# Optimization experiments

Measured on AMD Instinct MI355X. Metric: run time of the kernel, lower is better.

The kernel has to match this reference:

```python
import jax, jax.numpy as jnp
import numpy as np

N_A = 50000; N_B = 50000          # nodes per type
FD = 8; BINS = 32; EMB = 16       # discrete features, bins, per-feature embed dim
HID = 64; ZD = 32                 # hidden_dim, embed_dim
E = 800000                        # edges per relation (avg degree 16)


def setup_inputs() -> dict:
    key = jax.random.key(0)
    ks = iter(jax.random.split(key, 64))
    def nrm(shape, s=0.05):
        return jax.random.normal(next(ks), shape, jnp.float32) * s
    def ri(shape, hi):
        return jax.random.randint(next(ks), shape, 0, hi, dtype=jnp.int32)
    inp = {
        'x_A': ri((N_A, FD), BINS),
        'x_B': ri((N_B, FD), BINS),
        'ei_ab': ri((2, E), N_A),   # src in A, dst in B (N_A == N_B)
        'ei_ba': ri((2, E), N_B),
        'ei_aa': ri((2, E), N_A),
        # per-feature embedding tables [FD, BINS, EMB]
        'emb_A': nrm((FD, BINS, EMB)), 'emb_B': nrm((FD, BINS, EMB)),
        # pre_lin per node type (in = FD*EMB)
        'pre_W_A': nrm((FD * EMB, HID)), 'pre_b_A': nrm((HID,)),
        'pre_W_B': nrm((FD * EMB, HID)), 'pre_b_B': nrm((HID,)),
        # SAGEConv per relation: lin_l (on aggregated msgs, with bias), lin_r (root, no bias)
        'sage_l_W_ab': nrm((HID, HID)), 'sage_l_b_ab': nrm((HID,)), 'sage_r_W_ab': nrm((HID, HID)),
        'sage_l_W_ba': nrm((HID, HID)), 'sage_l_b_ba': nrm((HID,)), 'sage_r_W_ba': nrm((HID, HID)),
        'sage_l_W_aa': nrm((HID, HID)), 'sage_l_b_aa': nrm((HID,)), 'sage_r_W_aa': nrm((HID, HID)),
        # lin_proj per node type
        'proj_W_A': nrm((HID, ZD)), 'proj_b_A': nrm((ZD,)),
        'proj_W_B': nrm((HID, ZD)), 'proj_b_B': nrm((ZD,)),
        # feature heads per node type -> FD*BINS logits
        'head_W_A': nrm((ZD, FD * BINS)), 'head_b_A': nrm((FD * BINS,)),
        'head_W_B': nrm((ZD, FD * BINS)), 'head_b_B': nrm((FD * BINS,)),
        # bilinear edge decoders per relation: W [1, ZD, ZD], bias [1]
        'bil_W_ab': nrm((1, ZD, ZD)), 'bil_b_ab': nrm((1,)),
        'bil_W_ba': nrm((1, ZD, ZD)), 'bil_b_ba': nrm((1,)),
        'bil_W_aa': nrm((1, ZD, ZD)), 'bil_b_aa': nrm((1,)),
    }
    return inp


def _segment_mean(vals, idx, n):
    s = jax.ops.segment_sum(vals, idx, num_segments=n)
    c = jax.ops.segment_sum(jnp.ones((vals.shape[0], 1), vals.dtype), idx, num_segments=n)
    return s / jnp.maximum(c, 1.0)


def _sage(x_src, x_dst, ei, Wl, bl, Wr):
    # SAGEConv: lin_l(mean_{j in N(i)} x_j) + lin_r(x_i)
    m = _segment_mean(x_src[ei[0]], ei[1], x_dst.shape[0])
    return m @ Wl + bl + x_dst @ Wr


def _embed(x, emb):
    # emb: [FD, BINS, EMB]; x: [N, FD] ints -> [N, FD*EMB]
    e = emb[jnp.arange(FD)[None, :], x]            # [N, FD, EMB]
    return e.reshape(x.shape[0], FD * EMB)


def _bilinear(zs, zd, W, b):
    # nn.Bilinear: out_o = zs^T W_o zd + b_o ; here out dim 1, squeeze
    return (jnp.einsum('ei,oij,ej->eo', zs, W, zd) + b)[:, 0]


def _forward(x_A, x_B, ei_ab, ei_ba, ei_aa,
             emb_A, emb_B, pre_W_A, pre_b_A, pre_W_B, pre_b_B,
             sage_l_W_ab, sage_l_b_ab, sage_r_W_ab,
             sage_l_W_ba, sage_l_b_ba, sage_r_W_ba,
             sage_l_W_aa, sage_l_b_aa, sage_r_W_aa,
             proj_W_A, proj_b_A, proj_W_B, proj_b_B,
             head_W_A, head_b_A, head_W_B, head_b_B,
             bil_W_ab, bil_b_ab, bil_W_ba, bil_b_ba, bil_W_aa, bil_b_aa):
    # feature encoder + pre_lin + relu
    x0_A = jax.nn.relu(_embed(x_A, emb_A) @ pre_W_A + pre_b_A)
    x0_B = jax.nn.relu(_embed(x_B, emb_B) @ pre_W_B + pre_b_B)
    # HeteroConv(SAGEConv per relation, aggr='mean' over relations per dst type)
    h_B = _sage(x0_A, x0_B, ei_ab, sage_l_W_ab, sage_l_b_ab, sage_r_W_ab)
    h_A = (_sage(x0_B, x0_A, ei_ba, sage_l_W_ba, sage_l_b_ba, sage_r_W_ba)
           + _sage(x0_A, x0_A, ei_aa, sage_l_W_aa, sage_l_b_aa, sage_r_W_aa)) * 0.5
    # projection
    z_A = jax.nn.relu(h_A @ proj_W_A + proj_b_A)
    z_B = jax.nn.relu(h_B @ proj_W_B + proj_b_B)
    # feature decode
    fl_A = (z_A @ head_W_A + head_b_A).reshape(-1, FD, BINS)
    fl_B = (z_B @ head_W_B + head_b_B).reshape(-1, FD, BINS)
    # edge decode (bilinear on gathered endpoint embeddings)
    s_ab = _bilinear(z_A[ei_ab[0]], z_B[ei_ab[1]], bil_W_ab, bil_b_ab)
    s_ba = _bilinear(z_B[ei_ba[0]], z_A[ei_ba[1]], bil_W_ba, bil_b_ba)
    s_aa = _bilinear(z_A[ei_aa[0]], z_A[ei_aa[1]], bil_W_aa, bil_b_aa)
    return (z_A, z_B, fl_A, fl_B, s_ab, s_ba, s_aa)


def reference(x_A, x_B, ei_ab, ei_ba, ei_aa,
              emb_A, emb_B, pre_W_A, pre_b_A, pre_W_B, pre_b_B,
              sage_l_W_ab, sage_l_b_ab, sage_r_W_ab,
              sage_l_W_ba, sage_l_b_ba, sage_r_W_ba,
              sage_l_W_aa, sage_l_b_aa, sage_r_W_aa,
              proj_W_A, proj_b_A, proj_W_B, proj_b_B,
              head_W_A, head_b_A, head_W_B, head_b_B,
              bil_W_ab, bil_b_ab, bil_W_ba, bil_b_ba, bil_W_aa, bil_b_aa):
    return _forward(x_A, x_B, ei_ab, ei_ba, ei_aa,
                    emb_A, emb_B, pre_W_A, pre_b_A, pre_W_B, pre_b_B,
                    sage_l_W_ab, sage_l_b_ab, sage_r_W_ab,
                    sage_l_W_ba, sage_l_b_ba, sage_r_W_ba,
                    sage_l_W_aa, sage_l_b_aa, sage_r_W_aa,
                    proj_W_A, proj_b_A, proj_W_B, proj_b_B,
                    head_W_A, head_b_A, head_W_B, head_b_B,
                    bil_W_ab, bil_b_ab, bil_W_ba, bil_b_ba, bil_W_aa, bil_b_aa)
```

## Files before the change

kernel.cpp:

```cpp
#include <hip/hip_runtime.h>

typedef unsigned short u16;
typedef unsigned int u32;
typedef __attribute__((ext_vector_type(8))) short short8;
typedef __attribute__((ext_vector_type(4))) float f32x4;

constexpr int NA = 50000, NB = 50000;
constexpr int EMB = 16, HID = 64;
constexpr int NE = 800000;
constexpr int NBKT = 782;
constexpr int CAPB = 1536;
constexpr int EPB = 2048;
constexpr int BPR = (NE + EPB - 1) / EPB;
constexpr int MSB = 3 * BPR;

#define MFMA16(a, b, c) __builtin_amdgcn_mfma_f32_16x16x32_bf16(a, b, c, 0, 0, 0)

__device__ inline u16 f2bf(float f) {
  u32 b = __float_as_uint(f);
  return (u16)((b + 0x7FFFu + ((b >> 16) & 1u)) >> 16);
}
__device__ inline float bfl(u32 u) { return __uint_as_float(u << 16); }
__device__ inline float bfh(u32 u) { return __uint_as_float(u & 0xFFFF0000u); }
__device__ inline float bfs(u16 u) { return __uint_as_float((u32)u << 16); }

__global__ void __launch_bounds__(256) k_pre(
    const float* __restrict__ embA, const float* __restrict__ embB,
    const float* __restrict__ preWA, const float* __restrict__ preWB,
    float* __restrict__ T,
    const float* __restrict__ Wr_ba, const float* __restrict__ Wr_aa,
    const float* __restrict__ Wl_ba, const float* __restrict__ Wl_aa,
    const float* __restrict__ Wl_ab, const float* __restrict__ Wr_ab,
    const float* __restrict__ bl_ba, const float* __restrict__ bl_aa,
    const float* __restrict__ projWA, const float* __restrict__ projWB,
    const float* __restrict__ headWA, const float* __restrict__ headWB,
    const float* __restrict__ bilW_ba, const float* __restrict__ bilW_aa,
    const float* __restrict__ bilW_ab,
    u16* __restrict__ frag, float* __restrict__ bhA,
    const int* __restrict__ ei_ab, const int* __restrict__ ei_ba,
    const int* __restrict__ ei_aa, int* __restrict__ gcur,
    u32* __restrict__ buckets) {
  __shared__ int hist[NBKT];
  __shared__ int wcur[NBKT];
  int blk = blockIdx.x;
  int t = threadIdx.x;

  if (blk < MSB) {
    int rel = blk / BPR;
    int lb = blk - rel * BPR;
    const int* ei = rel == 0 ? ei_ab : (rel == 1 ? ei_ba : ei_aa);
    int e0 = lb * EPB;
    int n = min(EPB, NE - e0);
    for (int i = t; i < NBKT; i += 256) hist[i] = 0;
    __syncthreads();
    for (int i = t; i < n; i += 256) {
      int dstn = ei[NE + e0 + i];
      atomicAdd(&hist[dstn >> 6], 1);
    }
    __syncthreads();
    for (int i = t; i < NBKT; i += 256) {
      int c = hist[i];
      wcur[i] = (c > 0) ? atomicAdd(&gcur[rel * NBKT + i], c) : 0;
    }
    __syncthreads();
    for (int i = t; i < n; i += 256) {
      int src = ei[e0 + i];
      int dstn = ei[NE + e0 + i];
      int b = dstn >> 6;
      int pos = atomicAdd(&wcur[b], 1);
      if (pos < CAPB)
        buckets[(size_t)(rel * NBKT + b) * CAPB + pos] =
            ((u32)src << 6) | (u32)(dstn & 63);
    }
    return;
  }

  if (blk < MSB + 128) {
    int id = (blk - MSB) * 256 + t;
    int type = id >> 14;
    int rem = id & 16383;
    int col = rem >> 8;
    int fdbin = rem & 255;
    int fd = fdbin >> 5;
    const float* emb = type ? embB : embA;
    const float* W = type ? preWB : preWA;
    const float* e = emb + fdbin * EMB;
    const float* w = W + (fd * EMB) * HID + col;
    float s = 0.f;
#pragma unroll
    for (int j = 0; j < EMB; ++j) s += e[j] * w[j * HID];
    T[id] = s;
    return;
  }

  int tid = (blk - MSB - 128) * 256 + t;
  if (tid >= 86 * 64) {
    int i = tid - 86 * 64;
    if (i < 64) bhA[i] = 0.5f * (bl_ba[i] + bl_aa[i]);
    return;
  }
  int f = tid >> 6, lane = tid & 63;
  int nidx = lane & 15, quad = lane >> 4;
  u16* dst = frag + (size_t)f * 512 + lane * 8;
#pragma unroll
  for (int j = 0; j < 8; ++j) {
    int kq = quad * 8 + j;
    float v;
    if (f < 24) {
      int s = f >> 2, nt = f & 3, k = s * 32 + kq, c = nt * 16 + nidx;
      v = (k < 64) ? 0.5f * (Wr_ba[k * 64 + c] + Wr_aa[k * 64 + c])
          : (k < 128) ? 0.5f * Wl_ba[(k - 64) * 64 + c]
                      : 0.5f * Wl_aa[(k - 128) * 64 + c];
    } else if (f < 28) {
      int g = f - 24, k = (g >> 1) * 32 + kq, c = (g & 1) * 16 + nidx;
      v = projWA[k * 32 + c];
    } else if (f < 44) {
      int c = (f - 28) * 16 + nidx;
      v = headWA[kq * 256 + c];
    } else if (f < 46) {
      int i2 = (f - 44) * 16 + nidx;
      v = bilW_ba[i2 * 32 + kq];
    } else if (f < 48) {
      int i2 = (f - 46) * 16 + nidx;
      v = bilW_aa[i2 * 32 + kq];
    } else if (f < 64) {
      int g = f - 48, s = g >> 2, nt = g & 3, k = s * 32 + kq, c = nt * 16 + nidx;
      v = (k < 64) ? Wr_ab[k * 64 + c] : Wl_ab[(k - 64) * 64 + c];
    } else if (f < 68) {
      int g = f - 64, k = (g >> 1) * 32 + kq, c = (g & 1) * 16 + nidx;
      v = projWB[k * 32 + c];
    } else if (f < 84) {
      int c = (f - 68) * 16 + nidx;
      v = headWB[kq * 256 + c];
    } else {
      int i2 = (f - 84) * 16 + nidx;
      v = bilW_ab[i2 * 32 + kq];
    }
    dst[j] = f2bf(v);
  }
}

__global__ void __launch_bounds__(256) k_x0(const int* __restrict__ xA,
                                            const int* __restrict__ xB,
                                            const float* __restrict__ T,
                                            const float* __restrict__ biasA,
                                            const float* __restrict__ biasB,
                                            u16* __restrict__ x0A,
                                            u16* __restrict__ x0B) {
  extern __shared__ float Tl[];
  int blk = blockIdx.x;
  int type = blk >= 782;
  int lb = type ? blk - 782 : blk;
  const int* x = type ? xB : xA;
  const float* Tt = T + (type ? 16384 : 0);
  const float* bias = type ? biasB : biasA;
  u16* x0 = type ? x0B : x0A;
  const int N = NA;

  const float4* Tg = (const float4*)Tt;
  float4* Ts = (float4*)Tl;
  for (int i = threadIdx.x; i < 4096; i += 256) {
    int col = i >> 6, b4 = i & 63;
    Ts[col * 64 + ((b4 + 2 * (col >> 4)) & 63)] = Tg[i];
  }
  __syncthreads();
  int t = threadIdx.x;
  int r = t >> 2, q = t & 3;
  int row = lb * 64 + r;
  bool valid = row < N;
  int arow = valid ? row : (N - 1);
  const int4* xp = (const int4*)(x + arow * 8);
  int4 xa = xp[0], xb = xp[1];
  int bins[8] = {xa.x, xa.y, xa.z, xa.w, xb.x, xb.y, xb.z, xb.w};
  int c0 = q * 16;
  float acc[16];
#pragma unroll
  for (int j = 0; j < 16; ++j) acc[j] = bias[c0 + j];
#pragma unroll
  for (int fd = 0; fd < 8; ++fd) {
    int sb = ((fd * 32 + bins[fd]) + 8 * q) & 255;
#pragma unroll
    for (int j = 0; j < 16; ++j) acc[j] += Tl[(c0 + j) * 256 + sb];
  }
  if (valid) {
    u32 p[8];
#pragma unroll
    for (int j = 0; j < 8; ++j) {
      u16 lo = f2bf(fmaxf(acc[2 * j], 0.f));
      u16 hi = f2bf(fmaxf(acc[2 * j + 1], 0.f));
      p[j] = (u32)lo | ((u32)hi << 16);
    }
    u32* o = (u32*)(x0 + (size_t)row * 64 + c0);
    *(uint4*)o = *(uint4*)&p[0];
    *((uint4*)o + 1) = *(uint4*)&p[4];
  }
}

__global__ void __launch_bounds__(256) k_meansort_all(
    const u32* __restrict__ buckets, const int* __restrict__ cur,
    const u16* __restrict__ x0A, const u16* __restrict__ x0B,
    u16* __restrict__ mab, u16* __restrict__ mba, u16* __restrict__ maa) {
  __shared__ u32 ebuf[CAPB];
  __shared__ u16 csr[CAPB];
  __shared__ int dcnt[64], doff[64], wcur[64];
  int blk = blockIdx.x;
  int rel = blk / NBKT;
  int lb = blk - rel * NBKT;
  int t = threadIdx.x;
  const u16* x0 = (rel == 1) ? x0B : x0A;
  u16* out = rel == 0 ? mab : (rel == 1 ? mba : maa);
  int n = min(cur[blk], CAPB);
  const u32* bk = buckets + (size_t)blk * CAPB;
  if (t < 64) dcnt[t] = 0;
  __syncthreads();
  for (int i = t; i < n; i += 256) {
    u32 v = bk[i];
    ebuf[i] = v;
    atomicAdd(&dcnt[v & 63], 1);
  }
  __syncthreads();
  if (t == 0) {
    int s = 0;
#pragma unroll
    for (int d = 0; d < 64; ++d) {
      doff[d] = s;
      wcur[d] = s;
      s += dcnt[d];
    }
  }
  __syncthreads();
  for (int i = t; i < n; i += 256) {
    u32 v = ebuf[i];
    int p = atomicAdd(&wcur[v & 63], 1);
    csr[p] = (u16)(v >> 6);
  }
  __syncthreads();
  int lane = t & 63, w = t >> 6;
  int g = lane >> 4;
  int dim4 = (lane & 15) * 4;
  int base = lb * 64;
  for (int c = 0; c < 4; ++c) {
    int dloc = w * 16 + c * 4 + g;
    int dstn = base + dloc;
    if (dstn < 50000) {
      int off = doff[dloc], deg = dcnt[dloc];
      float a0 = 0.f, a1 = 0.f, a2 = 0.f, a3 = 0.f;
      int i = 0;
      for (; i + 8 <= deg; i += 8) {
        uint2 v0 = *(const uint2*)(x0 + (size_t)csr[off + i] * 64 + dim4);
        uint2 v1 = *(const uint2*)(x0 + (size_t)csr[off + i + 1] * 64 + dim4);
        uint2 v2 = *(const uint2*)(x0 + (size_t)csr[off + i + 2] * 64 + dim4);
        uint2 v3 = *(const uint2*)(x0 + (size_t)csr[off + i + 3] * 64 + dim4);
        uint2 v4 = *(const uint2*)(x0 + (size_t)csr[off + i + 4] * 64 + dim4);
        uint2 v5 = *(const uint2*)(x0 + (size_t)csr[off + i + 5] * 64 + dim4);
        uint2 v6 = *(const uint2*)(x0 + (size_t)csr[off + i + 6] * 64 + dim4);
        uint2 v7 = *(const uint2*)(x0 + (size_t)csr[off + i + 7] * 64 + dim4);
        a0 += bfl(v0.x) + bfl(v1.x) + bfl(v2.x) + bfl(v3.x) +
              bfl(v4.x) + bfl(v5.x) + bfl(v6.x) + bfl(v7.x);
        a1 += bfh(v0.x) + bfh(v1.x) + bfh(v2.x) + bfh(v3.x) +
              bfh(v4.x) + bfh(v5.x) + bfh(v6.x) + bfh(v7.x);
        a2 += bfl(v0.y) + bfl(v1.y) + bfl(v2.y) + bfl(v3.y) +
              bfl(v4.y) + bfl(v5.y) + bfl(v6.y) + bfl(v7.y);
        a3 += bfh(v0.y) + bfh(v1.y) + bfh(v2.y) + bfh(v3.y) +
              bfh(v4.y) + bfh(v5.y) + bfh(v6.y) + bfh(v7.y);
      }
      for (; i + 4 <= deg; i += 4) {
        uint2 v0 = *(const uint2*)(x0 + (size_t)csr[off + i] * 64 + dim4);
        uint2 v1 = *(const uint2*)(x0 + (size_t)csr[off + i + 1] * 64 + dim4);
        uint2 v2 = *(const uint2*)(x0 + (size_t)csr[off + i + 2] * 64 + dim4);
        uint2 v3 = *(const uint2*)(x0 + (size_t)csr[off + i + 3] * 64 + dim4);
        a0 += bfl(v0.x) + bfl(v1.x) + bfl(v2.x) + bfl(v3.x);
        a1 += bfh(v0.x) + bfh(v1.x) + bfh(v2.x) + bfh(v3.x);
        a2 += bfl(v0.y) + bfl(v1.y) + bfl(v2.y) + bfl(v3.y);
        a3 += bfh(v0.y) + bfh(v1.y) + bfh(v2.y) + bfh(v3.y);
      }
      for (; i < deg; ++i) {
        uint2 v0 = *(const uint2*)(x0 + (size_t)csr[off + i] * 64 + dim4);
        a0 += bfl(v0.x);
        a1 += bfh(v0.x);
        a2 += bfl(v0.y);
        a3 += bfh(v0.y);
      }
      float inv = deg > 0 ? 1.f / (float)deg : 0.f;
      uint2 o;
      o.x = (u32)f2bf(a0 * inv) | ((u32)f2bf(a1 * inv) << 16);
      o.y = (u32)f2bf(a2 * inv) | ((u32)f2bf(a3 * inv) << 16);
      *(uint2*)(out + (size_t)dstn * 64 + dim4) = o;
    }
  }
}

template <int NS, int NY>
__device__ __forceinline__ void node_chain(
    const u16* __restrict__ x0, const u16* __restrict__ m1, const u16* __restrict__ m2,
    const u16* __restrict__ frag, int f1, int f2, int fy, int fh,
    const float* __restrict__ hbias, const float* __restrict__ projb,
    const float* __restrict__ headb,
    float* __restrict__ zout, float* __restrict__ flout,
    u16* __restrict__ zbf, u16* __restrict__ y1bf, u16* __restrict__ y2bf,
    int rows0, int N, u16* hld, u16* zld, int lane) {
  int nidx = lane & 15, quad = lane >> 4;
  size_t r0 = (size_t)min(rows0 + nidx, N - 1);
  size_t r1 = (size_t)min(rows0 + 16 + nidx, N - 1);

  f32x4 acc[2][4];
#pragma unroll
  for (int mt = 0; mt < 2; ++mt)
#pragma unroll
    for (int nt = 0; nt < 4; ++nt) acc[mt][nt] = {0.f, 0.f, 0.f, 0.f};
  const u16* mats[3] = {x0, m1, m2};
#pragma unroll
  for (int s = 0; s < NS; ++s) {
    const u16* src = mats[s >> 1];
    int koff = (s & 1) * 32 + quad * 8;
    short8 a0 = *(const short8*)(src + r0 * 64 + koff);
    short8 a1 = *(const short8*)(src + r1 * 64 + koff);
#pragma unroll
    for (int nt = 0; nt < 4; ++nt) {
      short8 b = *(const short8*)(frag + (size_t)(f1 + s * 4 + nt) * 512 + lane * 8);
      acc[0][nt] = MFMA16(a0, b, acc[0][nt]);
      acc[1][nt] = MFMA16(a1, b, acc[1][nt]);
    }
  }
#pragma unroll
  for (int mt = 0; mt < 2; ++mt)
#pragma unroll
    for (int nt = 0; nt < 4; ++nt) {
      int col = nt * 16 + nidx;
      float bb = hbias[col];
#pragma unroll
      for (int r2 = 0; r2 < 4; ++r2)
        hld[(mt * 16 + quad * 4 + r2) * 72 + col] = f2bf(acc[mt][nt][r2] + bb);
    }

  f32x4 zacc[2][2];
#pragma unroll
  for (int mt = 0; mt < 2; ++mt)
#pragma unroll
    for (int nt = 0; nt < 2; ++nt) zacc[mt][nt] = {0.f, 0.f, 0.f, 0.f};
#pragma unroll
  for (int s = 0; s < 2; ++s) {
    short8 a0 = *(const short8*)(hld + nidx * 72 + s * 32 + quad * 8);
    short8 a1 = *(const short8*)(hld + (16 + nidx) * 72 + s * 32 + quad * 8);
#pragma unroll
    for (int nt = 0; nt < 2; ++nt) {
      short8 b = *(const short8*)(frag + (size_t)(f2 + s * 2 + nt) * 512 + lane * 8);
      zacc[0][nt] = MFMA16(a0, b, zacc[0][nt]);
      zacc[1][nt] = MFMA16(a1, b, zacc[1][nt]);
    }
  }
#pragma unroll
  for (int mt = 0; mt < 2; ++mt)
#pragma unroll
    for (int nt = 0; nt < 2; ++nt) {
      int col = nt * 16 + nidx;
      float pb = projb[col];
#pragma unroll
      for (int r2 = 0; r2 < 4; ++r2) {
        int rl = mt * 16 + quad * 4 + r2;
        float zv = fmaxf(zacc[mt][nt][r2] + pb, 0.f);
        zld[rl * 40 + col] = f2bf(zv);
        int grow = rows0 + rl;
        if (grow < N) zout[(size_t)grow * 32 + col] = zv;
      }
    }
  {
    int rl = lane >> 1, hf = lane & 1;
    int grow = rows0 + rl;
    if (grow < N) {
      short8 v0 = *(const short8*)(zld + rl * 40 + hf * 16);
      short8 v1 = *(const short8*)(zld + rl * 40 + hf * 16 + 8);
      *(short8*)(zbf + (size_t)grow * 32 + hf * 16) = v0;
      *(short8*)(zbf + (size_t)grow * 32 + hf * 16 + 8) = v1;
    }
  }

  short8 az0 = *(const short8*)(zld + nidx * 40 + quad * 8);
  short8 az1 = *(const short8*)(zld + (16 + nidx) * 40 + quad * 8);
#pragma unroll
  for (int mat = 0; mat < NY; ++mat) {
    f32x4 ya[2][2];
#pragma unroll
    for (int mt = 0; mt < 2; ++mt)
#pragma unroll
      for (int nt = 0; nt < 2; ++nt) ya[mt][nt] = {0.f, 0.f, 0.f, 0.f};
#pragma unroll
    for (int nt = 0; nt < 2; ++nt) {
      short8 b = *(const short8*)(frag + (size_t)(fy + mat * 2 + nt) * 512 + lane * 8);
      ya[0][nt] = MFMA16(az0, b, ya[0][nt]);
      ya[1][nt] = MFMA16(az1, b, ya[1][nt]);
    }
#pragma unroll
    for (int mt = 0; mt < 2; ++mt)
#pragma unroll
      for (int nt = 0; nt < 2; ++nt)
#pragma unroll
        for (int r2 = 0; r2 < 4; ++r2)
          hld[(mt * 16 + quad * 4 + r2) * 40 + nt * 16 + nidx] = f2bf(ya[mt][nt][r2]);
    u16* yo = mat ? y2bf : y1bf;
    int rl = lane >> 1, hf = lane & 1;
    int grow = rows0 + rl;
    if (grow < N) {
      short8 v0 = *(const short8*)(hld + rl * 40 + hf * 16);
      short8 v1 = *(const short8*)(hld + rl * 40 + hf * 16 + 8);
      *(short8*)(yo + (size_t)grow * 32 + hf * 16) = v0;
      *(short8*)(yo + (size_t)grow * 32 + hf * 16 + 8) = v1;
    }
  }

  for (int chunk = 0; chunk < 4; ++chunk) {
    f32x4 fa[2][4];
#pragma unroll
    for (int mt = 0; mt < 2; ++mt)
#pragma unroll
      for (int nt = 0; nt < 4; ++nt) fa[mt][nt] = {0.f, 0.f, 0.f, 0.f};
#pragma unroll
    for (int nt = 0; nt < 4; ++nt) {
      short8 b = *(const short8*)(frag + (size_t)(fh + chunk * 4 + nt) * 512 + lane * 8);
      fa[0][nt] = MFMA16(az0, b, fa[0][nt]);
      fa[1][nt] = MFMA16(az1, b, fa[1][nt]);
    }
#pragma unroll
    for (int mt = 0; mt < 2; ++mt)
#pragma unroll
      for (int nt = 0; nt < 4; ++nt) {
        int col = chunk * 64 + nt * 16 + nidx;
        float hb = headb[col];
#pragma unroll
        for (int r2 = 0; r2 < 4; ++r2) {
          int grow = rows0 + mt * 16 + quad * 4 + r2;
          if (grow < N) flout[(size_t)grow * 256 + col] = fa[mt][nt][r2] + hb;
        }
      }
  }
}

__global__ void __launch_bounds__(256) k_node(
    const u16* __restrict__ x0A, const u16* __restrict__ mba, const u16* __restrict__ maa,
    const u16* __restrict__ x0B, const u16* __restrict__ mab,
    const u16* __restrict__ frag, const float* __restrict__ bhA,
    const float* __restrict__ bl_ab,
    const float* __restrict__ projbA, const float* __restrict__ headbA,
    const float* __restrict__ projbB, const float* __restrict__ headbB,
    float* __restrict__ zA, float* __restrict__ flA, u16* __restrict__ zAbf,
    u16* __restrict__ ybabf, u16* __restrict__ yaabf,
    float* __restrict__ zB, float* __restrict__ flB, u16* __restrict__ zBbf,
    u16* __restrict__ yabbf) {
  __shared__ u16 lds[4][3584];
  int t = threadIdx.x, lane = t & 63, w = t >> 6;
  u16* hld = &lds[w][0];
  u16* zld = &lds[w][2304];
  int blk = blockIdx.x;
  if (blk < 391) {
    node_chain<6, 2>(x0A, mba, maa, frag, 0, 24, 44, 28, bhA, projbA, headbA,
                     zA, flA, zAbf, ybabf, yaabf, blk * 128 + w * 32, NA, hld, zld, lane);
  } else {
    node_chain<4, 1>(x0B, mab, mab, frag, 48, 64, 84, 68, bl_ab, projbB, headbB,
                     zB, flB, zBbf, yabbf, yabbf, (blk - 391) * 128 + w * 32, NB, hld,
                     zld, lane);
  }
}

__global__ void __launch_bounds__(256) k_bil_all(
    const int* __restrict__ ei_ab, const int* __restrict__ ei_ba,
    const int* __restrict__ ei_aa,
    const u16* __restrict__ zA, const u16* __restrict__ zB,
    const u16* __restrict__ yab, const u16* __restrict__ yba,
    const u16* __restrict__ yaa,
    const float* __restrict__ b_ab, const float* __restrict__ b_ba,
    const float* __restrict__ b_aa,
    float* __restrict__ s_ab, float* __restrict__ s_ba,
    float* __restrict__ s_aa) {
  constexpr int NCHUNK = NE / 256;
  int blk = blockIdx.x;
  int c = blk & 7;
  int o = blk >> 3;
  int rel, cb, ncls;
  if (c < 3) { rel = 0; cb = 0; ncls = 3; }
  else if (c < 6) { rel = 1; cb = 3; ncls = 3; }
  else { rel = 2; cb = 6; ncls = 2; }
  int chunk = (c - cb) + ncls * o;
  if (chunk >= NCHUNK) return;
  int le = chunk * 256 + threadIdx.x;
  const int* ei = rel == 0 ? ei_ab : (rel == 1 ? ei_ba : ei_aa);
  const u16* zs = (rel == 1) ? zB : zA;
  const u16* yd = rel == 0 ? yab : (rel == 1 ? yba : yaa);
  const float* bb = rel == 0 ? b_ab : (rel == 1 ? b_ba : b_aa);
  float* so = rel == 0 ? s_ab : (rel == 1 ? s_ba : s_aa);
  int si = ei[le], di = ei[NE + le];
  const uint4* zp = (const uint4*)(zs + (size_t)si * 32);
  const uint4* yp = (const uint4*)(yd + (size_t)di * 32);
  float acc = 0.f;
#pragma unroll
  for (int i = 0; i < 4; ++i) {
    uint4 a = zp[i], cc = yp[i];
    acc += bfl(a.x) * bfl(cc.x) + bfh(a.x) * bfh(cc.x);
    acc += bfl(a.y) * bfl(cc.y) + bfh(a.y) * bfh(cc.y);
    acc += bfl(a.z) * bfl(cc.z) + bfh(a.z) * bfh(cc.z);
    acc += bfl(a.w) * bfl(cc.w) + bfh(a.w) * bfh(cc.w);
  }
  so[le] = acc + bb[0];
}

extern "C" void kernel_launch(void* const* d_in, const int* in_sizes, int n_in,
                              void* d_out, int out_size, void* d_ws, size_t ws_size,
                              hipStream_t stream) {
  const int* xA = (const int*)d_in[0];
  const int* xB = (const int*)d_in[1];
  const int* ei_ab = (const int*)d_in[2];
  const int* ei_ba = (const int*)d_in[3];
  const int* ei_aa = (const int*)d_in[4];
  const float* embA = (const float*)d_in[5];
  const float* embB = (const float*)d_in[6];
  const float* preWA = (const float*)d_in[7];
  const float* prebA = (const float*)d_in[8];
  const float* preWB = (const float*)d_in[9];
  const float* prebB = (const float*)d_in[10];
  const float* Wl_ab = (const float*)d_in[11];
  const float* bl_ab = (const float*)d_in[12];
  const float* Wr_ab = (const float*)d_in[13];
  const float* Wl_ba = (const float*)d_in[14];
  const float* bl_ba = (const float*)d_in[15];
  const float* Wr_ba = (const float*)d_in[16];
  const float* Wl_aa = (const float*)d_in[17];
  const float* bl_aa = (const float*)d_in[18];
  const float* Wr_aa = (const float*)d_in[19];
  const float* projWA = (const float*)d_in[20];
  const float* projbA = (const float*)d_in[21];
  const float* projWB = (const float*)d_in[22];
  const float* projbB = (const float*)d_in[23];
  const float* headWA = (const float*)d_in[24];
  const float* headbA = (const float*)d_in[25];
  const float* headWB = (const float*)d_in[26];
  const float* headbB = (const float*)d_in[27];
  const float* bilW_ab = (const float*)d_in[28];
  const float* bilb_ab = (const float*)d_in[29];
  const float* bilW_ba = (const float*)d_in[30];
  const float* bilb_ba = (const float*)d_in[31];
  const float* bilW_aa = (const float*)d_in[32];
  const float* bilb_aa = (const float*)d_in[33];

  float* out = (float*)d_out;
  float* zA = out;
  float* zB = out + 1600000;
  float* flA = out + 3200000;
  float* flB = out + 16000000;
  float* s_ab = out + 28800000;
  float* s_ba = out + 29600000;
  float* s_aa = out + 30400000;

  char* ws = (char*)d_ws;
  float* T = (float*)(ws + 0);
  u16* x0Abf = (u16*)(ws + 131072);
  u16* x0Bbf = (u16*)(ws + 6531072);
  u16* mabbf = (u16*)(ws + 12931072);
  u16* mbabf = (u16*)(ws + 19331072);
  u16* maabf = (u16*)(ws + 25731072);
  u16* zAbf = (u16*)(ws + 32131072);
  u16* zBbf = (u16*)(ws + 35331072);
  u16* yabbf = (u16*)(ws + 38531072);
  u16* ybabf = (u16*)(ws + 41731072);
  u16* yaabf = (u16*)(ws + 44931072);
  int* cur = (int*)(ws + 48131072);
  u16* frag = (u16*)(ws + 48731072);
  float* bhA = (float*)(ws + 48819136);

  u32* buckets = (u32*)flA;

  hipMemsetAsync(cur, 0, 3 * NBKT * sizeof(int), stream);
  k_pre<<<MSB + 150, 256, 0, stream>>>(
      embA, embB, preWA, preWB, T,
      Wr_ba, Wr_aa, Wl_ba, Wl_aa, Wl_ab, Wr_ab, bl_ba, bl_aa,
      projWA, projWB, headWA, headWB, bilW_ba, bilW_aa, bilW_ab,
      frag, bhA, ei_ab, ei_ba, ei_aa, cur, buckets);
  k_x0<<<2 * 782, 256, 65536, stream>>>(xA, xB, T, prebA, prebB, x0Abf, x0Bbf);
  k_meansort_all<<<3 * NBKT, 256, 0, stream>>>(buckets, cur, x0Abf, x0Bbf,
                                               mabbf, mbabf, maabf);
  k_node<<<782, 256, 0, stream>>>(x0Abf, mbabf, maabf, x0Bbf, mabbf, frag, bhA,
                                  bl_ab, projbA, headbA, projbB, headbB,
                                  zA, flA, zAbf, ybabf, yaabf, zB, flB, zBbf, yabbf);
  k_bil_all<<<8 * 1563, 256, 0, stream>>>(
      ei_ab, ei_ba, ei_aa, zAbf, zBbf, yabbf, ybabf, yaabf,
      bilb_ab, bilb_ba, bilb_aa, s_ab, s_ba, s_aa);
}
```

Measured before the change: 411.4 us.

## Move edge bucketing into x0 kernel and enlarge edges per block

Moves the edge-bucketing blocks out of the small weight-prep kernel and into the x0 embedding kernel, so the bucketing runs alongside the x0 computation instead of before it. Raises edges per bucketing block from 2048 to 8192, which cuts the number of global cursor atomics and histogram passes. The cost is that every bucketing block now reserves the 64 KB dynamic shared memory, which can limit occupancy, and there are fewer, longer blocks that may leave a tail.

New measurement: 406.3 us. About the same (-1.2%).

```diff
diff --git a/kernel.cpp b/kernel.cpp
--- a/kernel.cpp
+++ b/kernel.cpp
@@ -10,7 +10,7 @@
 constexpr int NE = 800000;
 constexpr int NBKT = 782;
 constexpr int CAPB = 1536;
-constexpr int EPB = 2048;
+constexpr int EPB = 8192;
 constexpr int BPR = (NE + EPB - 1) / EPB;
 constexpr int MSB = 3 * BPR;
 
@@ -36,47 +36,12 @@
     const float* __restrict__ headWA, const float* __restrict__ headWB,
     const float* __restrict__ bilW_ba, const float* __restrict__ bilW_aa,
     const float* __restrict__ bilW_ab,
-    u16* __restrict__ frag, float* __restrict__ bhA,
-    const int* __restrict__ ei_ab, const int* __restrict__ ei_ba,
-    const int* __restrict__ ei_aa, int* __restrict__ gcur,
-    u32* __restrict__ buckets) {
-  __shared__ int hist[NBKT];
-  __shared__ int wcur[NBKT];
+    u16* __restrict__ frag, float* __restrict__ bhA) {
   int blk = blockIdx.x;
   int t = threadIdx.x;
 
-  if (blk < MSB) {
-    int rel = blk / BPR;
-    int lb = blk - rel * BPR;
-    const int* ei = rel == 0 ? ei_ab : (rel == 1 ? ei_ba : ei_aa);
-    int e0 = lb * EPB;
-    int n = min(EPB, NE - e0);
-    for (int i = t; i < NBKT; i += 256) hist[i] = 0;
-    __syncthreads();
-    for (int i = t; i < n; i += 256) {
-      int dstn = ei[NE + e0 + i];
-      atomicAdd(&hist[dstn >> 6], 1);
-    }
-    __syncthreads();
-    for (int i = t; i < NBKT; i += 256) {
-      int c = hist[i];
-      wcur[i] = (c > 0) ? atomicAdd(&gcur[rel * NBKT + i], c) : 0;
-    }
-    __syncthreads();
-    for (int i = t; i < n; i += 256) {
-      int src = ei[e0 + i];
-      int dstn = ei[NE + e0 + i];
-      int b = dstn >> 6;
-      int pos = atomicAdd(&wcur[b], 1);
-      if (pos < CAPB)
-        buckets[(size_t)(rel * NBKT + b) * CAPB + pos] =
-            ((u32)src << 6) | (u32)(dstn & 63);
-    }
-    return;
-  }
-
-  if (blk < MSB + 128) {
-    int id = (blk - MSB) * 256 + t;
+  if (blk < 128) {
+    int id = blk * 256 + t;
     int type = id >> 14;
     int rem = id & 16383;
     int col = rem >> 8;
@@ -93,7 +58,7 @@
     return;
   }
 
-  int tid = (blk - MSB - 128) * 256 + t;
+  int tid = (blk - 128) * 256 + t;
   if (tid >= 86 * 64) {
     int i = tid - 86 * 64;
     if (i < 64) bhA[i] = 0.5f * (bl_ba[i] + bl_aa[i]);
@@ -140,17 +105,54 @@
   }
 }
 
-__global__ void __launch_bounds__(256) k_x0(const int* __restrict__ xA,
-                                            const int* __restrict__ xB,
-                                            const float* __restrict__ T,
-                                            const float* __restrict__ biasA,
-                                            const float* __restrict__ biasB,
-                                            u16* __restrict__ x0A,
-                                            u16* __restrict__ x0B) {
-  extern __shared__ float Tl[];
+__global__ void __launch_bounds__(256) k_x0ms(
+    const int* __restrict__ xA, const int* __restrict__ xB,
+    const float* __restrict__ T,
+    const float* __restrict__ biasA, const float* __restrict__ biasB,
+    u16* __restrict__ x0A, u16* __restrict__ x0B,
+    const int* __restrict__ ei_ab, const int* __restrict__ ei_ba,
+    const int* __restrict__ ei_aa, int* __restrict__ gcur,
+    u32* __restrict__ buckets) {
+  extern __shared__ char smem[];
   int blk = blockIdx.x;
-  int type = blk >= 782;
-  int lb = type ? blk - 782 : blk;
+  int t = threadIdx.x;
+
+  if (blk < MSB) {
+    int* hist = (int*)smem;
+    int* wcur = hist + NBKT;
+    int rel = blk / BPR;
+    int lb = blk - rel * BPR;
+    const int* ei = rel == 0 ? ei_ab : (rel == 1 ? ei_ba : ei_aa);
+    int e0 = lb * EPB;
+    int n = min(EPB, NE - e0);
+    for (int i = t; i < NBKT; i += 256) hist[i] = 0;
+    __syncthreads();
+    for (int i = t; i < n; i += 256) {
+      int dstn = ei[NE + e0 + i];
+      atomicAdd(&hist[dstn >> 6], 1);
+    }
+    __syncthreads();
+    for (int i = t; i < NBKT; i += 256) {
+      int c = hist[i];
+      wcur[i] = (c > 0) ? atomicAdd(&gcur[rel * NBKT + i], c) : 0;
+    }
+    __syncthreads();
+    for (int i = t; i < n; i += 256) {
+      int src = ei[e0 + i];
+      int dstn = ei[NE + e0 + i];
+      int b = dstn >> 6;
+      int pos = atomicAdd(&wcur[b], 1);
+      if (pos < CAPB)
+        buckets[(size_t)(rel * NBKT + b) * CAPB + pos] =
+            ((u32)src << 6) | (u32)(dstn & 63);
+    }
+    return;
+  }
+
+  float* Tl = (float*)smem;
+  int xblk = blk - MSB;
+  int type = xblk >= 782;
+  int lb = type ? xblk - 782 : xblk;
   const int* x = type ? xB : xA;
   const float* Tt = T + (type ? 16384 : 0);
   const float* bias = type ? biasB : biasA;
@@ -159,12 +161,11 @@
 
   const float4* Tg = (const float4*)Tt;
   float4* Ts = (float4*)Tl;
-  for (int i = threadIdx.x; i < 4096; i += 256) {
+  for (int i = t; i < 4096; i += 256) {
     int col = i >> 6, b4 = i & 63;
     Ts[col * 64 + ((b4 + 2 * (col >> 4)) & 63)] = Tg[i];
   }
   __syncthreads();
-  int t = threadIdx.x;
   int r = t >> 2, q = t & 3;
   int row = lb * 64 + r;
   bool valid = row < N;
@@ -568,12 +569,14 @@
   u32* buckets = (u32*)flA;
 
   hipMemsetAsync(cur, 0, 3 * NBKT * sizeof(int), stream);
-  k_pre<<<MSB + 150, 256, 0, stream>>>(
+  k_pre<<<150, 256, 0, stream>>>(
       embA, embB, preWA, preWB, T,
       Wr_ba, Wr_aa, Wl_ba, Wl_aa, Wl_ab, Wr_ab, bl_ba, bl_aa,
       projWA, projWB, headWA, headWB, bilW_ba, bilW_aa, bilW_ab,
-      frag, bhA, ei_ab, ei_ba, ei_aa, cur, buckets);
-  k_x0<<<2 * 782, 256, 65536, stream>>>(xA, xB, T, prebA, prebB, x0Abf, x0Bbf);
+      frag, bhA);
+  k_x0ms<<<MSB + 2 * 782, 256, 65536, stream>>>(
+      xA, xB, T, prebA, prebB, x0Abf, x0Bbf,
+      ei_ab, ei_ba, ei_aa, cur, buckets);
   k_meansort_all<<<3 * NBKT, 256, 0, stream>>>(buckets, cur, x0Abf, x0Bbf,
                                                mabbf, mbabf, maabf);
   k_node<<<782, 256, 0, stream>>>(x0Abf, mbabf, maabf, x0Bbf, mabbf, frag, bhA,
```
